# Performance work log

Hardware: AMD Instinct MI355X
Metric: run time of the kernel (lower is better)

## Reference

```python
import jax, jax.numpy as jnp
import numpy as np

N = 100000          # nodes
F_IN = 500          # num_features
HID = 256           # hidden
C = 40              # out_classes
E = 2302585         # ~ N*ln(N)*ec, doubled (both directions) in spar_samp
ALPHA0 = 0.1        # att[0][0] = alpha*(1-alpha)**0


def setup_inputs() -> dict:
    key = jax.random.key(0)
    ks = jax.random.split(key, 8)
    x = jax.random.normal(ks[0], (N, F_IN), dtype=jnp.float32)
    W1 = jax.random.normal(ks[1], (F_IN, HID), dtype=jnp.float32) * (1.0 / np.sqrt(F_IN))
    b1 = jnp.zeros((HID,), dtype=jnp.float32)
    W2 = jax.random.normal(ks[2], (HID, C), dtype=jnp.float32) * (1.0 / np.sqrt(HID))
    b2 = jnp.zeros((C,), dtype=jnp.float32)
    edge_row = jax.random.randint(ks[3], (E,), 0, N, dtype=jnp.int64) if jax.config.jax_enable_x64 else jax.random.randint(ks[3], (E,), 0, N, dtype=jnp.int32)
    edge_col = jax.random.randint(ks[4], (E,), 0, N, dtype=edge_row.dtype)
    # sampled importance weights: deg^{-1/2}*deg^{-1/2}*(M/num_edgess) -> small positive floats
    edge_val = jax.random.uniform(ks[5], (E,), dtype=jnp.float32, minval=0.001, maxval=0.05)
    return {"x": x, "W1": W1, "b1": b1, "W2": W2, "b2": b2,
            "edge_row": edge_row, "edge_col": edge_col, "edge_val": edge_val}


def reference(x, W1, b1, W2, b2, edge_row, edge_col, edge_val):
    # eval mode: dropout is identity
    h = jax.nn.relu(x @ W1 + b1)          # [N, HID]
    h = h @ W2 + b2                       # [N, C]
    # sparse propagation: out[r] += val * h[c]  (scatter-add SpMM)
    msg = edge_val[:, None] * h[edge_col]            # [E, C] gather
    agg = jax.ops.segment_sum(msg, edge_row, num_segments=N)  # [N, C]
    out = h * ALPHA0 + agg
    return jax.nn.log_softmax(out, axis=1)
```

## Files before the change

kernel.cpp:

```cpp
#include <hip/hip_runtime.h>
#include <hip/hip_bf16.h>


#define N_NODES 100000
#define F_IN    500
#define HID     256
#define C_OUT   40
#define ALPHA0  0.1f
#define H2STRIDE 64

#define RPB     64
#define NBUCK   ((N_NODES + RPB - 1) / RPB)
#define NBUCKP  1568
#define NCH     256
#define BCAPL   1792

typedef short short8 __attribute__((ext_vector_type(8)));
typedef float f32x4  __attribute__((ext_vector_type(4)));

__device__ __forceinline__ short f2bf(float f) {
  union { float f; unsigned u; } x; x.f = f;
  unsigned r = x.u + 0x7fffu + ((x.u >> 16) & 1u);
  return (short)(r >> 16);
}
__device__ __forceinline__ float bf2f(short s) {
  union { unsigned u; float f; } x; x.u = ((unsigned)(unsigned short)s) << 16;
  return x.f;
}
__device__ __forceinline__ unsigned cvtpk(float lo, float hi) {
  unsigned r;
  asm("v_cvt_pk_bf16_f32 %0, %1, %2" : "=v"(r) : "v"(lo), "v"(hi));
  return r;
}
__device__ __forceinline__ void lbar() {
  asm volatile("s_waitcnt lgkmcnt(0)" ::: "memory");
  __builtin_amdgcn_s_barrier();
}
__device__ __forceinline__ void gll16(const float* g, const char* l) {
  __builtin_amdgcn_global_load_lds(
      (const __attribute__((address_space(1))) void*)g,
      (__attribute__((address_space(3))) void*)l, 16, 0, 0);
}

__global__ __launch_bounds__(256) void k_pack_weights(
    const float* __restrict__ W1, const float* __restrict__ W2,
    short* __restrict__ W1S, short* __restrict__ W2T)
{
  int i = blockIdx.x * 256 + threadIdx.x;
  if (i < 16*256*32) {
    int kc  = i >> 13;
    int idx = i & 8191;
    int n   = idx >> 5;
    int kk  = idx & 31;
    int k   = kc*32 + kk;
    float v = (k < F_IN) ? W1[k*HID + n] : 0.f;
    W1S[i] = f2bf(v);
  } else {
    int j = i - 16*256*32;
    if (j < 48*256) {
      int n = j >> 8;
      int k = j & 255;
      float v = (n < C_OUT) ? W2[k*C_OUT + n] : 0.f;
      W2T[j] = f2bf(v);
    }
  }
}

__global__ __launch_bounds__(256, 4) void k_fused_mlp(
    const float* __restrict__ x, const float* __restrict__ b1v,
    const float* __restrict__ b2v,
    const short* __restrict__ W1S, const short* __restrict__ W2T,
    short* __restrict__ h2b,
    const int* __restrict__ erow, int* __restrict__ lofs, int E, int CH)
{
  __shared__ __align__(16) char smem[32768];
  short (*Hl)[256] = (short(*)[256])smem;

  const int tid  = threadIdx.x;
  const int w    = tid >> 6;
  const int lane = tid & 63;
  const int lr   = lane & 15;
  const int quad = lane >> 4;
  const int row0 = blockIdx.x * 64;

  const int s_rl0 = (w*2)*8 + (lane>>3);
  const int s_rl1 = (w*2+1)*8 + (lane>>3);
  const int ksw   = ((lane&7) ^ ((lane>>3)&7)) * 4;
  const float* gp0 = x + (size_t)min(row0 + s_rl0, N_NODES-1) * F_IN;
  const float* gp1 = x + (size_t)min(row0 + s_rl1, N_NODES-1) * F_IN;
  const char* l0 = smem + (w*2)*1024;
  const char* l1 = smem + (w*2+1)*1024;

  f32x4 acc[4][4] = {};

  #pragma unroll
  for (int p = 0; p < 2; ++p) {
    int kb = p*32 + ksw;
    const float* a0 = (kb + 4 <= F_IN) ? gp0 + kb : x;
    const float* a1 = (kb + 4 <= F_IN) ? gp1 + kb : x;
    gll16(a0, l0 + p*8192);
    gll16(a1, l1 + p*8192);
  }

  const short* bbase = W1S + (w*64 + lr)*32 + quad*8;
  const int m2 = lr & 7;

  #pragma unroll
  for (int kc = 0; kc < 16; ++kc) {
    short8 bf4[4];
    #pragma unroll
    for (int t = 0; t < 4; ++t)
      bf4[t] = *(const short8*)(bbase + kc*8192 + t*16*32);
    __builtin_amdgcn_sched_barrier(0);

    if (kc < 14) {
      int kb = (kc+2)*32 + ksw;
      const float* a0 = (kb + 4 <= F_IN) ? gp0 + kb : x;
      const float* a1 = (kb + 4 <= F_IN) ? gp1 + kb : x;
      gll16(a0, l0 + ((kc+2)&3)*8192);
      gll16(a1, l1 + ((kc+2)&3)*8192);
      __builtin_amdgcn_sched_barrier(0);
      asm volatile("s_waitcnt vmcnt(8)" ::: "memory");
    } else if (kc == 14) {
      asm volatile("s_waitcnt vmcnt(6)" ::: "memory");
    } else {
      asm volatile("s_waitcnt vmcnt(4)" ::: "memory");
    }
    __builtin_amdgcn_s_barrier();

    const char* Abase = smem + (kc & 3)*8192;
    short8 af[4];
    #pragma unroll
    for (int t = 0; t < 4; ++t) {
      int rl = t*16 + lr;
      f32x4 u0 = *(const f32x4*)(Abase + rl*128 + (((quad*2  ) ^ m2) << 4));
      f32x4 u1 = *(const f32x4*)(Abase + rl*128 + (((quad*2+1) ^ m2) << 4));
      union { unsigned u[4]; short8 s; } pk;
      pk.u[0] = cvtpk(u0[0], u0[1]);
      pk.u[1] = cvtpk(u0[2], u0[3]);
      pk.u[2] = cvtpk(u1[0], u1[1]);
      pk.u[3] = cvtpk(u1[2], u1[3]);
      af[t] = pk.s;
    }

    #pragma unroll
    for (int rt = 0; rt < 4; ++rt)
      #pragma unroll
      for (int ct = 0; ct < 4; ++ct)
        acc[rt][ct] = __builtin_amdgcn_mfma_f32_16x16x32_bf16(af[rt], bf4[ct], acc[rt][ct], 0, 0, 0);
  }
  lbar();

  #pragma unroll
  for (int ct = 0; ct < 4; ++ct) {
    int col = w*64 + ct*16 + lr;
    int cg = col >> 3, ci = col & 7;
    float bias = b1v[col];
    #pragma unroll
    for (int rt = 0; rt < 4; ++rt) {
      #pragma unroll
      for (int r = 0; r < 4; ++r) {
        int row = rt*16 + quad*4 + r;
        float v = fmaxf(acc[rt][ct][r] + bias, 0.f);
        Hl[row][((cg ^ (row & 31)) << 3) | ci] = f2bf(v);
      }
    }
  }
  lbar();

  f32x4 acc2[3] = {};
  const int arow = w*16 + lr;
  #pragma unroll
  for (int kc2 = 0; kc2 < 8; ++kc2) {
    int gg = kc2*4 + quad;
    short8 a2 = *(const short8*)&Hl[arow][(gg ^ (arow & 31)) << 3];
    #pragma unroll
    for (int nt = 0; nt < 3; ++nt) {
      short8 b2 = *(const short8*)(W2T + (nt*16 + lr)*256 + kc2*32 + quad*8);
      acc2[nt] = __builtin_amdgcn_mfma_f32_16x16x32_bf16(a2, b2, acc2[nt], 0, 0, 0);
    }
  }

  #pragma unroll
  for (int nt = 0; nt < 3; ++nt) {
    int col = nt*16 + lr;
    float bias = (col < C_OUT) ? b2v[col] : 0.f;
    #pragma unroll
    for (int r = 0; r < 4; ++r) {
      int row = row0 + w*16 + quad*4 + r;
      if (row < N_NODES) {
        float v = (col < C_OUT) ? (acc2[nt][r] + bias) : 0.f;
        h2b[(long)row * H2STRIDE + col] = f2bf(v);
      }
    }
  }
  {
    int col = 48 + lr;
    #pragma unroll
    for (int r = 0; r < 4; ++r) {
      int row = row0 + w*16 + quad*4 + r;
      if (row < N_NODES) h2b[(long)row * H2STRIDE + col] = 0;
    }
  }

  if (blockIdx.x < NCH) {
    int cc = blockIdx.x;
    int* hcnt = (int*)smem;
    int* ssum = (int*)(smem + NBUCKP * 4);
    lbar();
    for (int b = tid; b < NBUCKP; b += 256) hcnt[b] = 0;
    __syncthreads();
    int e0 = cc * CH, e1 = min(E, e0 + CH);
    if (e0 < e1) {
      int g0 = e0 >> 2, g1 = e1 >> 2;
      const int4* rp = (const int4*)erow;
      for (int g = g0 + tid; g < g1; g += 256) {
        int4 r4 = rp[g];
        atomicAdd(&hcnt[r4.x >> 6], 1);
        atomicAdd(&hcnt[r4.y >> 6], 1);
        atomicAdd(&hcnt[r4.z >> 6], 1);
        atomicAdd(&hcnt[r4.w >> 6], 1);
      }
      for (int e = (g1 << 2) + tid; e < e1; e += 256)
        atomicAdd(&hcnt[erow[e] >> 6], 1);
    }
    __syncthreads();
    int base = tid * 8;
    int d[8];
    int s = 0;
    #pragma unroll
    for (int k = 0; k < 8; ++k) {
      d[k] = (base + k < NBUCKP) ? hcnt[base + k] : 0;
      s += d[k];
    }
    ssum[tid] = s;
    __syncthreads();
    for (int o = 1; o < 256; o <<= 1) {
      int u = (tid >= o) ? ssum[tid - o] : 0;
      __syncthreads();
      if (tid >= o) ssum[tid] += u;
      __syncthreads();
    }
    int run = ssum[tid] - s;
    #pragma unroll
    for (int k = 0; k < 8; ++k) {
      if (base + k < NBUCKP) lofs[(size_t)cc * NBUCKP + base + k] = run;
      run += d[k];
    }
  }
}

__global__ __launch_bounds__(256) void k_transpose(
    const int* __restrict__ lofs, int* __restrict__ lofsT)
{
  __shared__ int t[64][65];
  int cb = blockIdx.x & 3;
  int bb = blockIdx.x >> 2;
  int c0 = cb * 64, b0 = bb * 64;
  int j  = threadIdx.x & 63;
  int i0 = threadIdx.x >> 6;
  #pragma unroll
  for (int k = 0; k < 16; ++k) {
    int i = i0 + k * 4;
    int b = b0 + j;
    t[i][j] = (b <= NBUCK) ? lofs[(size_t)(c0 + i) * NBUCKP + b] : 0;
  }
  __syncthreads();
  #pragma unroll
  for (int k = 0; k < 16; ++k) {
    int i = i0 + k * 4;
    int b = b0 + i;
    if (b <= NBUCK) lofsT[(size_t)b * NCH + c0 + j] = t[j][i];
  }
}

__global__ __launch_bounds__(512) void k_split(
    const int* __restrict__ erow, const int* __restrict__ ecol,
    const float* __restrict__ eval, const int* __restrict__ lofs,
    int2* __restrict__ sorted, int E, int CH)
{
  __shared__ int cur[NBUCK];
  int tid = threadIdx.x, c = blockIdx.x;

  for (int b = tid; b < NBUCK; b += 512)
    cur[b] = lofs[(size_t)c * NBUCKP + b];
  __syncthreads();

  size_t obase = (size_t)c * CH;
  int e0 = c * CH, e1 = min(E, e0 + CH);
  if (e0 >= e1) return;
  int g0 = e0 >> 2, g1 = e1 >> 2;
  const int4*   rp = (const int4*)erow;
  const int4*   cp = (const int4*)ecol;
  const float4* vp = (const float4*)eval;
  for (int g = g0 + tid; g < g1; g += 512) {
    int4 r4 = rp[g];
    int4 c4 = cp[g];
    float4 v4 = vp[g];
    int p0 = atomicAdd(&cur[r4.x >> 6], 1);
    int p1 = atomicAdd(&cur[r4.y >> 6], 1);
    int p2 = atomicAdd(&cur[r4.z >> 6], 1);
    int p3 = atomicAdd(&cur[r4.w >> 6], 1);
    int2 cv;
    cv.x = c4.x | ((r4.x & 63) << 17); cv.y = __float_as_int(v4.x); sorted[obase + p0] = cv;
    cv.x = c4.y | ((r4.y & 63) << 17); cv.y = __float_as_int(v4.y); sorted[obase + p1] = cv;
    cv.x = c4.z | ((r4.z & 63) << 17); cv.y = __float_as_int(v4.z); sorted[obase + p2] = cv;
    cv.x = c4.w | ((r4.w & 63) << 17); cv.y = __float_as_int(v4.w); sorted[obase + p3] = cv;
  }
  for (int e = (g1 << 2) + tid; e < e1; e += 512) {
    int r = erow[e];
    int pos = atomicAdd(&cur[r >> 6], 1);
    int2 cv;
    cv.x = ecol[e] | ((r & 63) << 17);
    cv.y = __float_as_int(eval[e]);
    sorted[obase + pos] = cv;
  }
}

__global__ __launch_bounds__(512) void k_csr_spmm(
    const int* __restrict__ lofsT, const int2* __restrict__ sorted,
    const short* __restrict__ h2b, float* __restrict__ out, int CH)
{
  __shared__ int2 eraw[BCAPL];
  __shared__ int2 eS[BCAPL];
  __shared__ int sA[NCH];
  __shared__ int cntc[NCH];
  __shared__ int cpos[NCH];
  __shared__ int h[RPB], roff[RPB], cur[RPB];
  int tid = threadIdx.x, b = blockIdx.x;
  int lane = tid & 63, w = tid >> 6;

  if (tid < NCH) {
    int a  = lofsT[(size_t)b * NCH + tid];
    int e2 = lofsT[(size_t)(b + 1) * NCH + tid];
    sA[tid]   = a;
    cntc[tid] = e2 - a;
    cpos[tid] = e2 - a;
  }
  if (tid < RPB) h[tid] = 0;
  __syncthreads();
  for (int o = 1; o < NCH; o <<= 1) {
    int u = (tid >= o && tid < NCH) ? cpos[tid - o] : 0;
    __syncthreads();
    if (tid >= o && tid < NCH) cpos[tid] += u;
    __syncthreads();
  }
  int cntT = min(cpos[NCH - 1], BCAPL);

  {
    int c    = tid & (NCH - 1);
    int half = tid >> 8;
    int srcb = c * CH + sA[c];
    int dstb = cpos[c] - cntc[c];
    int n    = cntc[c];
    for (int k = half; k < n; k += 2) {
      int p = dstb + k;
      if (p < BCAPL) {
        int2 cv = sorted[srcb + k];
        eraw[p] = cv;
        atomicAdd(&h[((unsigned)cv.x) >> 17], 1);
      }
    }
  }
  __syncthreads();
  if (w == 0) {
    int v = h[lane];
    int hv = v;
    #pragma unroll
    for (int o = 1; o < 64; o <<= 1) {
      int t = __shfl_up(v, o);
      if (lane >= o) v += t;
    }
    roff[lane] = v;
    cur[lane]  = v - hv;
  }
  __syncthreads();
  for (int i = tid; i < cntT; i += 512) {
    int2 cv = eraw[i];
    int p = atomicAdd(&cur[((unsigned)cv.x) >> 17], 1);
    if (p < BCAPL) eS[p] = cv;
  }
  __syncthreads();

  for (int rr = 0; rr < 8; ++rr) {
    int r = w * 8 + rr;
    int row = b * RPB + r;
    if (row >= N_NODES) continue;
    float acc = ALPHA0 * bf2f(h2b[(size_t)row * H2STRIDE + lane]);
    int e  = roff[r] - h[r];
    int ee = roff[r];
    for (; e + 7 < ee; e += 8) {
      int2 cc[8];
      float gg[8];
      #pragma unroll
      for (int j = 0; j < 8; ++j) cc[j] = eS[e + j];
      #pragma unroll
      for (int j = 0; j < 8; ++j)
        gg[j] = bf2f(h2b[(size_t)(cc[j].x & 0x1FFFF) * H2STRIDE + lane]);
      #pragma unroll
      for (int j = 0; j < 8; ++j) acc += __int_as_float(cc[j].y) * gg[j];
    }
    for (; e + 3 < ee; e += 4) {
      int2 c0 = eS[e], c1 = eS[e+1], c2 = eS[e+2], c3 = eS[e+3];
      float g0 = bf2f(h2b[(size_t)(c0.x & 0x1FFFF) * H2STRIDE + lane]);
      float g1 = bf2f(h2b[(size_t)(c1.x & 0x1FFFF) * H2STRIDE + lane]);
      float g2 = bf2f(h2b[(size_t)(c2.x & 0x1FFFF) * H2STRIDE + lane]);
      float g3 = bf2f(h2b[(size_t)(c3.x & 0x1FFFF) * H2STRIDE + lane]);
      acc += __int_as_float(c0.y) * g0;
      acc += __int_as_float(c1.y) * g1;
      acc += __int_as_float(c2.y) * g2;
      acc += __int_as_float(c3.y) * g3;
    }
    for (; e < ee; ++e) {
      int2 c0 = eS[e];
      acc += __int_as_float(c0.y) * bf2f(h2b[(size_t)(c0.x & 0x1FFFF) * H2STRIDE + lane]);
    }
    float m = (lane < C_OUT) ? acc : -INFINITY;
    #pragma unroll
    for (int o = 32; o > 0; o >>= 1) m = fmaxf(m, __shfl_xor(m, o));
    float ev = (lane < C_OUT) ? __expf(acc - m) : 0.f;
    float s = ev;
    #pragma unroll
    for (int o = 32; o > 0; o >>= 1) s += __shfl_xor(s, o);
    if (lane < C_OUT) out[(long)row * C_OUT + lane] = acc - m - __logf(s);
  }
}

extern "C" void kernel_launch(void* const* d_in, const int* in_sizes, int n_in,
                              void* d_out, int out_size, void* d_ws, size_t ws_size,
                              hipStream_t stream) {
  const float* x    = (const float*)d_in[0];
  const float* W1   = (const float*)d_in[1];
  const float* b1   = (const float*)d_in[2];
  const float* W2   = (const float*)d_in[3];
  const float* b2   = (const float*)d_in[4];
  const int*   erow = (const int*)d_in[5];
  const int*   ecol = (const int*)d_in[6];
  const float* eval = (const float*)d_in[7];
  const int E  = in_sizes[5];
  int CH = (E + NCH - 1) / NCH;
  CH = (CH + 3) & ~3;

  char* p = (char*)d_ws;
  short* h2b    = (short*)p;  p += (size_t)N_NODES * H2STRIDE * 2;
  short* W1S    = (short*)p;  p += (size_t)16*256*32 * 2;
  short* W2T    = (short*)p;  p += (size_t)48*256 * 2;
  int*   lofs   = (int*)p;    p += (size_t)NCH * NBUCKP * 4;
  int*   lofsT  = (int*)p;    p += (size_t)1600 * NCH * 4;
  int2*  sorted = (int2*)p;
  float* out = (float*)d_out;

  k_pack_weights<<<(16*256*32 + 48*256 + 255)/256, 256, 0, stream>>>(W1, W2, W1S, W2T);
  k_fused_mlp<<<(N_NODES + 63)/64, 256, 0, stream>>>(x, b1, b2, W1S, W2T, h2b,
                                                     erow, lofs, E, CH);
  k_transpose<<<4 * 25, 256, 0, stream>>>(lofs, lofsT);
  k_split<<<NCH, 512, 0, stream>>>(erow, ecol, eval, lofs, sorted, E, CH);
  k_csr_spmm<<<NBUCK, 512, 0, stream>>>(lofsT, sorted, h2b, out, CH);
}
```

Measured before the change: 457.0 us.

## Fuse edge bucket scatter into MLP kernel's histogram blocks, drop k_split

```diff
diff --git a/kernel.cpp b/kernel.cpp
--- a/kernel.cpp
+++ b/kernel.cpp
@@ -71,7 +71,9 @@
     const float* __restrict__ b2v,
     const short* __restrict__ W1S, const short* __restrict__ W2T,
     short* __restrict__ h2b,
-    const int* __restrict__ erow, int* __restrict__ lofs, int E, int CH)
+    const int* __restrict__ erow, const int* __restrict__ ecol,
+    const float* __restrict__ eval, int* __restrict__ lofs,
+    int2* __restrict__ sorted, int E, int CH)
 {
   __shared__ __align__(16) char smem[32768];
   short (*Hl)[256] = (short(*)[256])smem;
@@ -211,9 +213,9 @@
     for (int b = tid; b < NBUCKP; b += 256) hcnt[b] = 0;
     __syncthreads();
     int e0 = cc * CH, e1 = min(E, e0 + CH);
+    int g0 = e0 >> 2, g1 = e1 >> 2;
+    const int4* rp = (const int4*)erow;
     if (e0 < e1) {
-      int g0 = e0 >> 2, g1 = e1 >> 2;
-      const int4* rp = (const int4*)erow;
       for (int g = g0 + tid; g < g1; g += 256) {
         int4 r4 = rp[g];
         atomicAdd(&hcnt[r4.x >> 6], 1);
@@ -242,10 +244,45 @@
       __syncthreads();
     }
     int run = ssum[tid] - s;
+    int curv[8];
     #pragma unroll
     for (int k = 0; k < 8; ++k) {
+      curv[k] = run;
       if (base + k < NBUCKP) lofs[(size_t)cc * NBUCKP + base + k] = run;
       run += d[k];
+    }
+    __syncthreads();
+    #pragma unroll
+    for (int k = 0; k < 8; ++k)
+      if (base + k < NBUCKP) hcnt[base + k] = curv[k];
+    __syncthreads();
+
+    if (e0 < e1) {
+      size_t obase = (size_t)cc * CH;
+      const int4*   cp = (const int4*)ecol;
+      const float4* vp = (const float4*)eval;
+      for (int g = g0 + tid; g < g1; g += 256) {
+        int4 r4 = rp[g];
+        int4 c4 = cp[g];
+        float4 v4 = vp[g];
+        int p0 = atomicAdd(&hcnt[r4.x >> 6], 1);
+        int p1 = atomicAdd(&hcnt[r4.y >> 6], 1);
+        int p2 = atomicAdd(&hcnt[r4.z >> 6], 1);
+        int p3 = atomicAdd(&hcnt[r4.w >> 6], 1);
+        int2 cv;
+        cv.x = c4.x | ((r4.x & 63) << 17); cv.y = __float_as_int(v4.x); sorted[obase + p0] = cv;
+        cv.x = c4.y | ((r4.y & 63) << 17); cv.y = __float_as_int(v4.y); sorted[obase + p1] = cv;
+        cv.x = c4.z | ((r4.z & 63) << 17); cv.y = __float_as_int(v4.z); sorted[obase + p2] = cv;
+        cv.x = c4.w | ((r4.w & 63) << 17); cv.y = __float_as_int(v4.w); sorted[obase + p3] = cv;
+      }
+      for (int e = (g1 << 2) + tid; e < e1; e += 256) {
+        int r = erow[e];
+        int pos = atomicAdd(&hcnt[r >> 6], 1);
+        int2 cv;
+        cv.x = ecol[e] | ((r & 63) << 17);
+        cv.y = __float_as_int(eval[e]);
+        sorted[obase + pos] = cv;
+      }
     }
   }
 }
@@ -271,49 +308,6 @@
     int i = i0 + k * 4;
     int b = b0 + i;
     if (b <= NBUCK) lofsT[(size_t)b * NCH + c0 + j] = t[j][i];
-  }
-}
-
-__global__ __launch_bounds__(512) void k_split(
-    const int* __restrict__ erow, const int* __restrict__ ecol,
-    const float* __restrict__ eval, const int* __restrict__ lofs,
-    int2* __restrict__ sorted, int E, int CH)
-{
-  __shared__ int cur[NBUCK];
-  int tid = threadIdx.x, c = blockIdx.x;
-
-  for (int b = tid; b < NBUCK; b += 512)
-    cur[b] = lofs[(size_t)c * NBUCKP + b];
-  __syncthreads();
-
-  size_t obase = (size_t)c * CH;
-  int e0 = c * CH, e1 = min(E, e0 + CH);
-  if (e0 >= e1) return;
-  int g0 = e0 >> 2, g1 = e1 >> 2;
-  const int4*   rp = (const int4*)erow;
-  const int4*   cp = (const int4*)ecol;
-  const float4* vp = (const float4*)eval;
-  for (int g = g0 + tid; g < g1; g += 512) {
-    int4 r4 = rp[g];
-    int4 c4 = cp[g];
-    float4 v4 = vp[g];
-    int p0 = atomicAdd(&cur[r4.x >> 6], 1);
-    int p1 = atomicAdd(&cur[r4.y >> 6], 1);
-    int p2 = atomicAdd(&cur[r4.z >> 6], 1);
-    int p3 = atomicAdd(&cur[r4.w >> 6], 1);
-    int2 cv;
-    cv.x = c4.x | ((r4.x & 63) << 17); cv.y = __float_as_int(v4.x); sorted[obase + p0] = cv;
-    cv.x = c4.y | ((r4.y & 63) << 17); cv.y = __float_as_int(v4.y); sorted[obase + p1] = cv;
-    cv.x = c4.z | ((r4.z & 63) << 17); cv.y = __float_as_int(v4.z); sorted[obase + p2] = cv;
-    cv.x = c4.w | ((r4.w & 63) << 17); cv.y = __float_as_int(v4.w); sorted[obase + p3] = cv;
-  }
-  for (int e = (g1 << 2) + tid; e < e1; e += 512) {
-    int r = erow[e];
-    int pos = atomicAdd(&cur[r >> 6], 1);
-    int2 cv;
-    cv.x = ecol[e] | ((r & 63) << 17);
-    cv.y = __float_as_int(eval[e]);
-    sorted[obase + pos] = cv;
   }
 }
 
@@ -452,8 +446,8 @@
 
   k_pack_weights<<<(16*256*32 + 48*256 + 255)/256, 256, 0, stream>>>(W1, W2, W1S, W2T);
   k_fused_mlp<<<(N_NODES + 63)/64, 256, 0, stream>>>(x, b1, b2, W1S, W2T, h2b,
-                                                     erow, lofs, E, CH);
+                                                     erow, ecol, eval, lofs,
+                                                     sorted, E, CH);
   k_transpose<<<4 * 25, 256, 0, stream>>>(lofs, lofsT);
-  k_split<<<NCH, 512, 0, stream>>>(erow, ecol, eval, lofs, sorted, E, CH);
   k_csr_spmm<<<NBUCK, 512, 0, stream>>>(lofsT, sorted, h2b, out, CH);
 }
```

After: 457.2 us. No clear change (+0.0%).
